# Kernel optimization log

Hardware: AMD Instinct MI355X
Metric: run time of the kernel (lower is better)

Reference implementation:

```python
import jax, jax.numpy as jnp
import numpy as np

EPS = 1e-5  # torch BatchNorm default eps


def _bn(x, g, b, axes):
    # Training-mode batch norm (biased variance, as torch uses for normalization)
    m = x.mean(axes, keepdims=True)
    v = x.var(axes, keepdims=True)
    sh = [1] * x.ndim
    sh[1] = x.shape[1]
    return (x - m) / jnp.sqrt(v + EPS) * g.reshape(sh) + b.reshape(sh)


def _conv2d(x, w, b, pad):
    y = jax.lax.conv_general_dilated(x, w, (1, 1), ((pad, pad), (pad, pad)),
                                     dimension_numbers=('NCHW', 'OIHW', 'NCHW'))
    return y + b.reshape(1, -1, 1, 1)


def _conv3d(x, w, b):
    # kernel (1,1,3), padding (0,0,1)
    y = jax.lax.conv_general_dilated(x, w, (1, 1, 1), ((0, 0), (0, 0), (1, 1)),
                                     dimension_numbers=('NCDHW', 'OIDHW', 'NCDHW'))
    return y + b.reshape(1, -1, 1, 1, 1)


def _block(x, w, b, g, be):
    return jax.nn.relu(_bn(_conv2d(x, w, b, 1), g, be, (0, 2, 3)))


def _pool(x):
    return jax.lax.reduce_window(x, -jnp.inf, jax.lax.max, (1, 1, 2, 2), (1, 1, 2, 2), 'VALID')


def _interp_axis(x, axis):
    # bilinear, align_corners=True, scale factor 2 along one axis
    n = x.shape[axis]
    out = 2 * n
    pos = jnp.linspace(0.0, n - 1.0, out)
    lo = jnp.floor(pos).astype(jnp.int32)
    hi = jnp.minimum(lo + 1, n - 1)
    w = (pos - lo).astype(x.dtype)
    sh = [1] * x.ndim
    sh[axis] = out
    w = w.reshape(sh)
    return jnp.take(x, lo, axis=axis) * (1 - w) + jnp.take(x, hi, axis=axis) * w


def _upsample(x):
    return _interp_axis(_interp_axis(x, 2), 3)


def _forward(x, tp_w1, tp_b1, tp_g1, tp_be1, tp_w2, tp_b2, tp_g2, tp_be2,
             range_w, doppler_w,
             enc1_w, enc1_b, enc1_g, enc1_be,
             enc2_w, enc2_b, enc2_g, enc2_be,
             enc3_w, enc3_b, enc3_g, enc3_be,
             dec3_w, dec3_b, dec3_g, dec3_be,
             dec2_w, dec2_b, dec2_g, dec2_be,
             dec1_w, dec1_b, dec1_g, dec1_be,
             out_w, out_b):
    # x: [B, RX, C, S, 2] -> [B, 2, RX, C, S]
    h = jnp.transpose(x, (0, 4, 1, 2, 3))
    h = jax.nn.relu(_bn(_conv3d(h, tp_w1, tp_b1), tp_g1, tp_be1, (0, 2, 3, 4)))
    h = jax.nn.relu(_bn(_conv3d(h, tp_w2, tp_b2), tp_g2, tp_be2, (0, 2, 3, 4)))
    h = jnp.transpose(h, (0, 2, 3, 4, 1)).sum(axis=1)  # sum over RX -> [B, C, S, 2]
    xr, xi = h[..., 0], h[..., 1]
    # Range DFT (quadruple loop in torch == two complex matmuls)
    Wr, Wi = range_w[..., 0], range_w[..., 1]  # [S, R]
    rr = jnp.einsum('bcs,sr->bcr', xr, Wr) - jnp.einsum('bcs,sr->bcr', xi, Wi)
    ri = jnp.einsum('bcs,sr->bcr', xr, Wi) + jnp.einsum('bcs,sr->bcr', xi, Wr)
    # Doppler DFT over chirps
    Dr, Di = doppler_w[..., 0], doppler_w[..., 1]  # [C, D]
    rdr = jnp.einsum('bcr,cd->bdr', rr, Dr) - jnp.einsum('bcr,cd->bdr', ri, Di)
    rdi = jnp.einsum('bcr,cd->bdr', rr, Di) + jnp.einsum('bcr,cd->bdr', ri, Dr)
    rd = jnp.stack([rdr, rdi], axis=1)  # [B, 2, D, R]
    # RadarNet U-Net
    e1 = _block(rd, enc1_w, enc1_b, enc1_g, enc1_be)
    p1 = _pool(e1)
    e2 = _block(p1, enc2_w, enc2_b, enc2_g, enc2_be)
    p2 = _pool(e2)
    e3 = _block(p2, enc3_w, enc3_b, enc3_g, enc3_be)
    d3 = _block(e3, dec3_w, dec3_b, dec3_g, dec3_be)
    u2 = _upsample(d3) + e2
    d2 = _block(u2, dec2_w, dec2_b, dec2_g, dec2_be)
    u1 = _upsample(d2) + e1
    d1 = _block(u1, dec1_w, dec1_b, dec1_g, dec1_be)
    out = jax.nn.sigmoid(_conv2d(d1, out_w, out_b, 0))
    return jnp.transpose(out, (0, 2, 3, 1))  # [B, D, R, 1]


def setup_inputs() -> dict:
    key = jax.random.key(0)
    ctr = [0]

    def rn(shape, scale=1.0):
        ctr[0] += 1
        return jax.random.normal(jax.random.fold_in(key, ctr[0]), shape, dtype=jnp.float32) * scale

    B, RX, C, S, D, R = 16, 4, 128, 256, 128, 256
    inp = {
        'x': rn((B, RX, C, S, 2)),
        'tp_w1': rn((8, 2, 1, 1, 3), 0.4), 'tp_b1': jnp.zeros(8), 'tp_g1': jnp.ones(8), 'tp_be1': jnp.zeros(8),
        'tp_w2': rn((2, 8, 1, 1, 3), 0.2), 'tp_b2': jnp.zeros(2), 'tp_g2': jnp.ones(2), 'tp_be2': jnp.zeros(2),
        'range_w': rn((S, R, 2)), 'doppler_w': rn((C, D, 2)),
        'enc1_w': rn((32, 2, 3, 3), 0.1), 'enc1_b': jnp.zeros(32), 'enc1_g': jnp.ones(32), 'enc1_be': jnp.zeros(32),
        'enc2_w': rn((64, 32, 3, 3), 0.05), 'enc2_b': jnp.zeros(64), 'enc2_g': jnp.ones(64), 'enc2_be': jnp.zeros(64),
        'enc3_w': rn((128, 64, 3, 3), 0.04), 'enc3_b': jnp.zeros(128), 'enc3_g': jnp.ones(128), 'enc3_be': jnp.zeros(128),
        'dec3_w': rn((64, 128, 3, 3), 0.03), 'dec3_b': jnp.zeros(64), 'dec3_g': jnp.ones(64), 'dec3_be': jnp.zeros(64),
        'dec2_w': rn((32, 64, 3, 3), 0.04), 'dec2_b': jnp.zeros(32), 'dec2_g': jnp.ones(32), 'dec2_be': jnp.zeros(32),
        'dec1_w': rn((16, 32, 3, 3), 0.05), 'dec1_b': jnp.zeros(16), 'dec1_g': jnp.ones(16), 'dec1_be': jnp.zeros(16),
        'out_w': rn((1, 16, 1, 1), 0.25), 'out_b': jnp.zeros(1),
    }
    return inp


def reference(x, tp_w1, tp_b1, tp_g1, tp_be1, tp_w2, tp_b2, tp_g2, tp_be2,
              range_w, doppler_w,
              enc1_w, enc1_b, enc1_g, enc1_be,
              enc2_w, enc2_b, enc2_g, enc2_be,
              enc3_w, enc3_b, enc3_g, enc3_be,
              dec3_w, dec3_b, dec3_g, dec3_be,
              dec2_w, dec2_b, dec2_g, dec2_be,
              dec1_w, dec1_b, dec1_g, dec1_be,
              out_w, out_b):
    return _forward(x, tp_w1, tp_b1, tp_g1, tp_be1, tp_w2, tp_b2, tp_g2, tp_be2,
                    range_w, doppler_w,
                    enc1_w, enc1_b, enc1_g, enc1_be,
                    enc2_w, enc2_b, enc2_g, enc2_be,
                    enc3_w, enc3_b, enc3_g, enc3_be,
                    dec3_w, dec3_b, dec3_g, dec3_be,
                    dec2_w, dec2_b, dec2_g, dec2_be,
                    dec1_w, dec1_b, dec1_g, dec1_be,
                    out_w, out_b)
```

## Files before the change

### kernel.cpp

```cpp
#include <hip/hip_runtime.h>
#include <cmath>

constexpr int Bn = 16, RXn = 4, Cn = 128, Sn = 256, Dn = 128, Rn = 256;

typedef __attribute__((ext_vector_type(8))) short bf16x8;
typedef __attribute__((ext_vector_type(4))) float f32x4;
typedef unsigned short u16;
typedef unsigned int u32;
typedef __attribute__((ext_vector_type(4))) u16 u16x4;
typedef __attribute__((ext_vector_type(8))) u16 u16x8;
typedef __attribute__((ext_vector_type(2))) u32 u32x2;
typedef __attribute__((ext_vector_type(4))) u32 u32x4;

__device__ __forceinline__ u16 f2bf(float f) {
  union { float f; u32 u; } v; v.f = f;
  const u32 r = v.u + 0x7FFFu + ((v.u >> 16) & 1u);
  return (u16)(r >> 16);
}
__device__ __forceinline__ float bf2f(u16 h) {
  union { u32 u; float f; } v; v.u = (u32)h << 16; return v.f;
}
__device__ __forceinline__ u32 cvtpk(float lo, float hi) {
  u32 r;
  asm("v_cvt_pk_bf16_f32 %0, %1, %2" : "=v"(r) : "v"(lo), "v"(hi));
  return r;
}
__device__ __forceinline__ void split2(float a, float b, u32& hi, u32& lo) {
  hi = cvtpk(a, b);
  union { u32 u; float f; } va, vb;
  va.u = hi << 16;
  vb.u = hi & 0xFFFF0000u;
  lo = cvtpk(a - va.f, b - vb.f);
}
__device__ __forceinline__ void ld8bf(const u16* __restrict__ p, float* v) {
  const u16x8 h = *(const u16x8*)p;
#pragma unroll
  for (int k = 0; k < 8; ++k) v[k] = bf2f(h[k]);
}

__device__ __forceinline__ void pack_seg(const float* __restrict__ w, u16* __restrict__ wpk,
                                         int CIN, int COUT, int gid, int gsz) {
  const int total = COUT * CIN * 9;
  const int chunks = CIN >> 5;
  for (int idx = gid; idx < total; idx += gsz) {
    const int j = idx & 7;
    const int l = (idx >> 3) & 63;
    const int rest = idx >> 9;
    const int t = rest % 9;
    const int rest2 = rest / 9;
    const int q = rest2 % chunks;
    const int mf = rest2 / chunks;
    const int co = mf * 16 + (l & 15);
    const int ci = q * 32 + ((l >> 4) << 3) + j;
    wpk[idx] = f2bf(w[((size_t)co * CIN + ci) * 9 + t]);
  }
}

__global__ __launch_bounds__(256) void k_pack_stats(
    const float* __restrict__ e2w, const float* __restrict__ e3w,
    const float* __restrict__ d3w, const float* __restrict__ d2w,
    const float* __restrict__ d1w,
    const float* __restrict__ range_w, const float* __restrict__ dopp_w,
    u16* __restrict__ p_e2, u16* __restrict__ p_e3,
    u16* __restrict__ p_d3, u16* __restrict__ p_d2,
    u16* __restrict__ p_d1,
    u16* __restrict__ A1h, u16* __restrict__ A1l,
    u16* __restrict__ A2h, u16* __restrict__ A2l,
    const float* __restrict__ x, const float* __restrict__ w1,
    float* __restrict__ part) {
  if (blockIdx.x < 128) {
    const int gid = blockIdx.x * 256 + threadIdx.x;
    const int gsz = 128 * 256;
    pack_seg(e2w, p_e2, 32, 64, gid, gsz);
    pack_seg(e3w, p_e3, 64, 128, gid, gsz);
    pack_seg(d3w, p_d3, 128, 64, gid, gsz);
    pack_seg(d2w, p_d2, 64, 32, gid, gsz);
    pack_seg(d1w, p_d1, 32, 16, gid, gsz);
    for (int idx = gid; idx < 512 * 512; idx += gsz) {
      const int m = idx >> 9, k = idx & 511;
      const int r = m >> 1, p = m & 1, s = k >> 1, q = k & 1;
      const float Wr = range_w[((size_t)s * Rn + r) * 2 + 0];
      const float Wi = range_w[((size_t)s * Rn + r) * 2 + 1];
      const float v = (p == 0) ? ((q == 0) ? Wr : -Wi) : ((q == 0) ? Wi : Wr);
      const u16 h = f2bf(v);
      A1h[idx] = h;
      A1l[idx] = f2bf(v - bf2f(h));
    }
    for (int idx = gid; idx < 256 * 256; idx += gsz) {
      const int m = idx >> 8, k = idx & 255;
      const int d = m >> 1, p = m & 1, c = k >> 1, q = k & 1;
      const float Dr = dopp_w[((size_t)c * Dn + d) * 2 + 0];
      const float Di = dopp_w[((size_t)c * Dn + d) * 2 + 1];
      const float v = (p == 0) ? ((q == 0) ? Dr : -Di) : ((q == 0) ? Di : Dr);
      const u16 h = f2bf(v);
      A2h[idx] = h;
      A2l[idx] = f2bf(v - bf2f(h));
    }
    return;
  }
  const int bx = blockIdx.x - 128;
  __shared__ float w1s[48];
  __shared__ float red8[8][4][2];
  const int t = threadIdx.x;
  if (t < 48) w1s[t] = w1[t];
  __syncthreads();
  float s1[8], s2[8];
#pragma unroll
  for (int o = 0; o < 8; ++o) { s1[o] = 0.f; s2[o] = 0.f; }
  for (int row = bx; row < Bn * RXn * Cn; row += 1024) {
    const float* xr = x + (size_t)row * Sn * 2;
    const float2 cc = *(const float2*)&xr[2 * t];
    const float2 mm = (t > 0) ? *(const float2*)&xr[2 * t - 2] : make_float2(0.f, 0.f);
    const float2 pp = (t < Sn - 1) ? *(const float2*)&xr[2 * t + 2] : make_float2(0.f, 0.f);
#pragma unroll
    for (int o = 0; o < 8; ++o) {
      const float* w = &w1s[o * 6];
      float h = w[0] * mm.x + w[1] * cc.x + w[2] * pp.x + w[3] * mm.y + w[4] * cc.y + w[5] * pp.y;
      s1[o] += h; s2[o] += h * h;
    }
  }
  const int lane = t & 63, wv = t >> 6;
#pragma unroll
  for (int o = 0; o < 8; ++o) {
    float v1 = s1[o], v2 = s2[o];
#pragma unroll
    for (int off = 32; off; off >>= 1) { v1 += __shfl_down(v1, off); v2 += __shfl_down(v2, off); }
    if (lane == 0) { red8[o][wv][0] = v1; red8[o][wv][1] = v2; }
  }
  __syncthreads();
  if (t < 8) {
    const float a1 = red8[t][0][0] + red8[t][1][0] + red8[t][2][0] + red8[t][3][0];
    const float a2 = red8[t][0][1] + red8[t][1][1] + red8[t][2][1] + red8[t][3][1];
    part[((size_t)t * 1024 + bx) * 2 + 0] = a1;
    part[((size_t)t * 1024 + bx) * 2 + 1] = a2;
  }
}

__global__ __launch_bounds__(256) void k_finalize(const float* __restrict__ part, int npart,
                                                  float n, const float* __restrict__ g,
                                                  const float* __restrict__ be,
                                                  float* __restrict__ stats) {
  const int co = blockIdx.x, t = threadIdx.x;
  __shared__ float r1[256], r2[256];
  float s1 = 0.f, s2 = 0.f;
  for (int i = t; i < npart; i += 256) {
    s1 += part[((size_t)co * npart + i) * 2 + 0];
    s2 += part[((size_t)co * npart + i) * 2 + 1];
  }
  r1[t] = s1; r2[t] = s2;
  __syncthreads();
  for (int off = 128; off; off >>= 1) {
    if (t < off) { r1[t] += r1[t + off]; r2[t] += r2[t + off]; }
    __syncthreads();
  }
  if (t == 0) {
    const float mean = r1[0] / n;
    const float var  = fmaxf(r2[0] / n - mean * mean, 0.f);
    const float inv  = rsqrtf(var + 1e-5f);
    const float sc   = inv * g[co];
    stats[2 * co + 0] = sc;
    stats[2 * co + 1] = be[co] - mean * sc;
  }
}

__global__ __launch_bounds__(256) void k_tp_fused2(const float* __restrict__ x,
                                                   const float* __restrict__ w1,
                                                   const float* __restrict__ st1,
                                                   const float* __restrict__ w2,
                                                   u32* __restrict__ h2p,
                                                   float* __restrict__ part) {
  __shared__ float a1[8][Sn + 2];
  __shared__ float w1s[48], w2s[48], st[16];
  __shared__ float red2s[2][4][2];
  const int t = threadIdx.x;
  const int row = blockIdx.x;
  if (t < 48) { w1s[t] = w1[t]; w2s[t] = w2[t]; }
  if (t < 16) st[t] = st1[t];
  __syncthreads();
  const float* xr = x + (size_t)row * Sn * 2;
  const float2 cc = *(const float2*)&xr[2 * t];
  const float2 mm = (t > 0) ? *(const float2*)&xr[2 * t - 2] : make_float2(0.f, 0.f);
  const float2 pp = (t < Sn - 1) ? *(const float2*)&xr[2 * t + 2] : make_float2(0.f, 0.f);
#pragma unroll
  for (int o = 0; o < 8; ++o) {
    const float* w = &w1s[o * 6];
    float h = w[0] * mm.x + w[1] * cc.x + w[2] * pp.x + w[3] * mm.y + w[4] * cc.y + w[5] * pp.y;
    float v = fmaf(h, st[2 * o], st[2 * o + 1]);
    a1[o][1 + t] = v > 0.f ? v : 0.f;
    if (t == 0) { a1[o][0] = 0.f; a1[o][Sn + 1] = 0.f; }
  }
  __syncthreads();
  float h2v[2];
#pragma unroll
  for (int j = 0; j < 2; ++j) {
    float acc = 0.f;
#pragma unroll
    for (int o = 0; o < 8; ++o) {
      const float* w = &w2s[j * 24 + o * 3];
      acc += w[0] * a1[o][t] + w[1] * a1[o][t + 1] + w[2] * a1[o][t + 2];
    }
    h2v[j] = acc;
  }
  h2p[(size_t)row * Sn + t] = cvtpk(h2v[0], h2v[1]);
  const int lane = t & 63, wv = t >> 6;
#pragma unroll
  for (int j = 0; j < 2; ++j) {
    float v1 = h2v[j], v2 = h2v[j] * h2v[j];
#pragma unroll
    for (int off = 32; off; off >>= 1) { v1 += __shfl_down(v1, off); v2 += __shfl_down(v2, off); }
    if (lane == 0) { red2s[j][wv][0] = v1; red2s[j][wv][1] = v2; }
  }
  __syncthreads();
  if (t < 2) {
    const float a1s = red2s[t][0][0] + red2s[t][1][0] + red2s[t][2][0] + red2s[t][3][0];
    const float a2s = red2s[t][0][1] + red2s[t][1][1] + red2s[t][2][1] + red2s[t][3][1];
    part[((size_t)t * gridDim.x + row) * 2 + 0] = a1s;
    part[((size_t)t * gridDim.x + row) * 2 + 1] = a2s;
  }
}

__global__ __launch_bounds__(256) void k_prep(const u32* __restrict__ h2p,
                                              const float* __restrict__ st2,
                                              u32* __restrict__ B1h32,
                                              u32* __restrict__ B1l32) {
  const int row = blockIdx.x;
  const int s = threadIdx.x;
  const int b = row >> 7, c = row & (Cn - 1);
  const float sc0 = st2[0], sh0 = st2[1], sc1 = st2[2], sh1 = st2[3];
  float xr = 0.f, xi = 0.f;
#pragma unroll
  for (int rx = 0; rx < RXn; ++rx) {
    const u32 v = h2p[(((size_t)b * RXn + rx) * Cn + c) * Sn + s];
    const float vr = bf2f((u16)(v & 0xFFFFu));
    const float vi = bf2f((u16)(v >> 16));
    xr += fmaxf(fmaf(vr, sc0, sh0), 0.f);
    xi += fmaxf(fmaf(vi, sc1, sh1), 0.f);
  }
  u32 hi, lo;
  split2(xr, xi, hi, lo);
  B1h32[(size_t)row * 256 + s] = hi;
  B1l32[(size_t)row * 256 + s] = lo;
}

template <int M, int N, int K, int STORE>
__global__ __launch_bounds__(256) void k_gemm_split(const u16* __restrict__ Ah,
                                                    const u16* __restrict__ Al,
                                                    const u16* __restrict__ Bh,
                                                    const u16* __restrict__ Bl,
                                                    u32* __restrict__ out0,
                                                    u32* __restrict__ out1) {
  __shared__ __align__(16) u16 lah[32 * 40], lal[32 * 40];
  __shared__ __align__(16) u16 lbh[64 * 40], lbl[64 * 40];
  const int tid = threadIdx.x;
  const int lane = tid & 63, wid = tid >> 6;
  const int wm = wid >> 1, wn = wid & 1;
  const int l15 = lane & 15, lg = lane >> 4;
  const int m0 = blockIdx.x * 32, n0 = blockIdx.y * 64;
  f32x4 acc[2];
  acc[0] = (f32x4){0.f, 0.f, 0.f, 0.f};
  acc[1] = (f32x4){0.f, 0.f, 0.f, 0.f};
  const int arow = tid >> 3, ak = (tid & 7) * 4;
  const int brow = tid >> 2, bk = (tid & 3) * 8;
  for (int k0 = 0; k0 < K; k0 += 32) {
    *(u16x4*)&lah[arow * 40 + ak] = *(const u16x4*)&Ah[(size_t)(m0 + arow) * K + k0 + ak];
    *(u16x4*)&lal[arow * 40 + ak] = *(const u16x4*)&Al[(size_t)(m0 + arow) * K + k0 + ak];
    *(u16x8*)&lbh[brow * 40 + bk] = *(const u16x8*)&Bh[(size_t)(n0 + brow) * K + k0 + bk];
    *(u16x8*)&lbl[brow * 40 + bk] = *(const u16x8*)&Bl[(size_t)(n0 + brow) * K + k0 + bk];
    __syncthreads();
    const bf16x8 ah = *(const bf16x8*)&lah[(wm * 16 + l15) * 40 + lg * 8];
    const bf16x8 al = *(const bf16x8*)&lal[(wm * 16 + l15) * 40 + lg * 8];
#pragma unroll
    for (int f = 0; f < 2; ++f) {
      const bf16x8 bh = *(const bf16x8*)&lbh[(wn * 32 + f * 16 + l15) * 40 + lg * 8];
      const bf16x8 bl = *(const bf16x8*)&lbl[(wn * 32 + f * 16 + l15) * 40 + lg * 8];
      acc[f] = __builtin_amdgcn_mfma_f32_16x16x32_bf16(ah, bh, acc[f], 0, 0, 0);
      acc[f] = __builtin_amdgcn_mfma_f32_16x16x32_bf16(ah, bl, acc[f], 0, 0, 0);
      acc[f] = __builtin_amdgcn_mfma_f32_16x16x32_bf16(al, bh, acc[f], 0, 0, 0);
    }
    __syncthreads();
  }
  const int mb = m0 + wm * 16 + lg * 4;
#pragma unroll
  for (int f = 0; f < 2; ++f) {
    const int n = n0 + wn * 32 + f * 16 + l15;
    if (STORE == 0) {
      const int b = n >> 7, c = n & 127;
#pragma unroll
      for (int pair = 0; pair < 2; ++pair) {
        const int r = (mb >> 1) + pair;
        u32 hi, lo;
        split2(acc[f][2 * pair], acc[f][2 * pair + 1], hi, lo);
        const size_t idx = ((size_t)b * 256 + r) * 128 + c;
        out0[idx] = hi;
        out1[idx] = lo;
      }
    } else {
      const int b = n >> 8, r = n & 255;
#pragma unroll
      for (int pair = 0; pair < 2; ++pair) {
        const int d = (mb >> 1) + pair;
        out0[((size_t)b * 128 + d) * 256 + r] = cvtpk(acc[f][2 * pair], acc[f][2 * pair + 1]);
      }
    }
  }
}

template <int CIN, int COUT, int H, int W, int TH, int TW, int MW, int NW,
          int WAVES_M, int WAVES_N, int MODE>
__global__ __launch_bounds__(256) void k_conv_mfma(const u16* __restrict__ in,
                                                   const u16* __restrict__ wpk,
                                                   const float* __restrict__ in_stats,
                                                   const u16* __restrict__ in2,
                                                   const float* __restrict__ in2_stats,
                                                   u16* __restrict__ out,
                                                   float* __restrict__ part) {
  constexpr int COG = WAVES_M * MW * 16;
  constexpr int CHUNKS = CIN / 32;
  constexpr int NFROW = TW / 16;
  constexpr int XROWS = TH + 2, XCOLS = TW + 2;
  static_assert(WAVES_M * WAVES_N == 4, "waves");
  static_assert(WAVES_N * NW * 16 == TH * TW, "pixel cover");
  __shared__ __align__(16) u16 xs[XROWS * XCOLS * 40];
  __shared__ float red1[WAVES_N][COG], red2[WAVES_N][COG];
  __shared__ __align__(16) float sst1[2 * CIN];
  __shared__ __align__(16) float sst2[(MODE == 3) ? 2 * CIN : 4];
  const int tid = threadIdx.x;
  const int lane = tid & 63;
  const int wid = tid >> 6;
  const int wave_m = wid / WAVES_N;
  const int wave_n = wid % WAVES_N;
  const int l15 = lane & 15, lg = lane >> 4;
  constexpr int TILES_W = W / TW;
  const int tile = blockIdx.x;
  const int tw = tile % TILES_W, th = tile / TILES_W;
  const int h0 = th * TH, w0 = tw * TW;
  const int cog = blockIdx.y, b = blockIdx.z;
  for (int i = tid; i < 2 * CIN; i += 256) sst1[i] = in_stats[i];
  if (MODE == 3)
    for (int i = tid; i < 2 * CIN; i += 256) sst2[i] = in2_stats[i];
  __syncthreads();
  f32x4 acc[MW][NW];
#pragma unroll
  for (int m = 0; m < MW; ++m)
#pragma unroll
    for (int f = 0; f < NW; ++f) acc[m][f] = (f32x4){0.f, 0.f, 0.f, 0.f};

  for (int q = 0; q < CHUNKS; ++q) {
    for (int i = tid; i < XROWS * XCOLS * 4; i += 256) {
      const int ci0 = (i & 3) * 8;
      const int pix = i >> 2;
      const int col = pix % XCOLS;
      const int row = pix / XCOLS;
      const int gh = h0 + row - 1, gw = w0 + col - 1;
      const int cch = q * 32 + ci0;
      u32x4 enc = (u32x4){0u, 0u, 0u, 0u};
      if (gh >= 0 && gh < H && gw >= 0 && gw < W) {
        float vv[8];
        float sc[8], sh[8];
#pragma unroll
        for (int k = 0; k < 4; ++k) {
          const float4 qq = *(const float4*)&sst1[2 * cch + 4 * k];
          sc[2 * k] = qq.x; sh[2 * k] = qq.y; sc[2 * k + 1] = qq.z; sh[2 * k + 1] = qq.w;
        }
        if (MODE == 1) {
          float tv[8];
          ld8bf(&in[(((size_t)b * H + gh) * W + gw) * CIN + cch], tv);
#pragma unroll
          for (int k = 0; k < 8; ++k) vv[k] = fmaxf(fmaf(tv[k], sc[k], sh[k]), 0.f);
        } else if (MODE == 2) {
          const size_t rs = (size_t)(2 * W) * CIN;
          const u16* pb = &in[(((size_t)b * 2 * H + 2 * gh) * (2 * W) + 2 * gw) * CIN + cch];
          float tp[4][8];
          ld8bf(pb, tp[0]);
          ld8bf(pb + CIN, tp[1]);
          ld8bf(pb + rs, tp[2]);
          ld8bf(pb + rs + CIN, tp[3]);
#pragma unroll
          for (int k = 0; k < 8; ++k) {
            const float mx = fmaxf(fmaxf(tp[0][k], tp[1][k]), fmaxf(tp[2][k], tp[3][k]));
            vv[k] = fmaxf(fmaf(mx, sc[k], sh[k]), 0.f);
          }
        } else {
          constexpr int Hi2 = H / 2, Wi2 = W / 2;
          constexpr float steph = (float)(Hi2 - 1) / (float)(H - 1);
          constexpr float stepw = (float)(Wi2 - 1) / (float)(W - 1);
          const float ph = (float)gh * steph;
          const int hlo = (int)ph;
          const int hhi = (hlo + 1 < Hi2) ? hlo + 1 : Hi2 - 1;
          const float fh = ph - (float)hlo;
          const float pw = (float)gw * stepw;
          const int wl = (int)pw;
          const int wh = (wl + 1 < Wi2) ? wl + 1 : Wi2 - 1;
          const float fw = pw - (float)wl;
          const float w00 = (1.f - fh) * (1.f - fw), w01 = (1.f - fh) * fw;
          const float w10 = fh * (1.f - fw), w11 = fh * fw;
          const u16* dbase = &in[(size_t)b * Hi2 * Wi2 * CIN + cch];
          float tp[4][8];
          ld8bf(dbase + ((size_t)hlo * Wi2 + wl) * CIN, tp[0]);
          ld8bf(dbase + ((size_t)hlo * Wi2 + wh) * CIN, tp[1]);
          ld8bf(dbase + ((size_t)hhi * Wi2 + wl) * CIN, tp[2]);
          ld8bf(dbase + ((size_t)hhi * Wi2 + wh) * CIN, tp[3]);
          float ec[8], es[8];
#pragma unroll
          for (int k = 0; k < 4; ++k) {
            const float4 qq = *(const float4*)&sst2[2 * cch + 4 * k];
            ec[2 * k] = qq.x; es[2 * k] = qq.y; ec[2 * k + 1] = qq.z; es[2 * k + 1] = qq.w;
          }
          float ev[8];
          ld8bf(&in2[(((size_t)b * H + gh) * W + gw) * CIN + cch], ev);
#pragma unroll
          for (int k = 0; k < 8; ++k) {
            const float a = fmaxf(fmaf(tp[0][k], sc[k], sh[k]), 0.f);
            const float bb = fmaxf(fmaf(tp[1][k], sc[k], sh[k]), 0.f);
            const float cc = fmaxf(fmaf(tp[2][k], sc[k], sh[k]), 0.f);
            const float dd = fmaxf(fmaf(tp[3][k], sc[k], sh[k]), 0.f);
            vv[k] = w00 * a + w01 * bb + w10 * cc + w11 * dd
                  + fmaxf(fmaf(ev[k], ec[k], es[k]), 0.f);
          }
        }
#pragma unroll
        for (int j = 0; j < 4; ++j) enc[j] = cvtpk(vv[2 * j], vv[2 * j + 1]);
      }
      *(u32x4*)&xs[(row * XCOLS + col) * 40 + ci0] = enc;
    }
    __syncthreads();
#pragma unroll
    for (int t = 0; t < 9; ++t) {
      const int ky = t / 3, kx = t % 3;
      bf16x8 afr[MW];
#pragma unroll
      for (int m = 0; m < MW; ++m) {
        const int mfg = cog * (COG / 16) + wave_m * MW + m;
        afr[m] = *(const bf16x8*)&wpk[((((size_t)mfg * CHUNKS + q) * 9 + t) * 64 + lane) * 8];
      }
      bf16x8 bfr[NW];
#pragma unroll
      for (int f = 0; f < NW; ++f) {
        const int nf = wave_n * NW + f;
        const int r = nf / NFROW;
        const int cseg = (nf % NFROW) * 16;
        bfr[f] = *(const bf16x8*)&xs[((r + ky) * XCOLS + (cseg + l15 + kx)) * 40 + lg * 8];
      }
#pragma unroll
      for (int m = 0; m < MW; ++m)
#pragma unroll
        for (int f = 0; f < NW; ++f)
          acc[m][f] = __builtin_amdgcn_mfma_f32_16x16x32_bf16(afr[m], bfr[f], acc[m][f], 0, 0, 0);
    }
    __syncthreads();
  }

#pragma unroll
  for (int m = 0; m < MW; ++m) {
    const int cobase = cog * COG + (wave_m * MW + m) * 16 + lg * 4;
#pragma unroll
    for (int f = 0; f < NW; ++f) {
      const int nf = wave_n * NW + f;
      const int r = nf / NFROW;
      const int cseg = (nf % NFROW) * 16;
      u16* op = out + (((size_t)b * H + h0 + r) * W + (w0 + cseg + l15)) * COUT + cobase;
      u32x2 ov;
      ov[0] = cvtpk(acc[m][f][0], acc[m][f][1]);
      ov[1] = cvtpk(acc[m][f][2], acc[m][f][3]);
      *(u32x2*)op = ov;
    }
  }
#pragma unroll
  for (int m = 0; m < MW; ++m)
#pragma unroll
    for (int reg = 0; reg < 4; ++reg) {
      float s1 = 0.f, s2 = 0.f;
#pragma unroll
      for (int f = 0; f < NW; ++f) { const float v = acc[m][f][reg]; s1 += v; s2 += v * v; }
#pragma unroll
      for (int off = 1; off < 16; off <<= 1) { s1 += __shfl_xor(s1, off); s2 += __shfl_xor(s2, off); }
      if (l15 == 0) {
        const int ch = (wave_m * MW + m) * 16 + lg * 4 + reg;
        red1[wave_n][ch] = s1; red2[wave_n][ch] = s2;
      }
    }
  __syncthreads();
  if (tid < COG) {
    float s1 = 0.f, s2 = 0.f;
#pragma unroll
    for (int wn = 0; wn < WAVES_N; ++wn) { s1 += red1[wn][tid]; s2 += red2[wn][tid]; }
    const int npart = gridDim.x * gridDim.z;
    const int pidx = blockIdx.z * gridDim.x + blockIdx.x;
    part[((size_t)(cog * COG + tid) * npart + pidx) * 2 + 0] = s1;
    part[((size_t)(cog * COG + tid) * npart + pidx) * 2 + 1] = s2;
  }
}

__global__ __launch_bounds__(256) void k_conv1(const u32* __restrict__ in,
                                               const float* __restrict__ wgt,
                                               u16* __restrict__ out,
                                               float* __restrict__ part) {
  constexpr int H = 128, W = 256, TW = 64, TH = 16, COG = 16, COUT = 32;
  const int tid = threadIdx.x;
  const int tile = blockIdx.x;
  const int tw = tile & 3, th = tile >> 2;
  const int cog = blockIdx.y, b = blockIdx.z;
  const int ty = tid >> 4;
  const int wofs = (tid & 15) * 4;
  const int h0 = th * TH, w0t = tw * TW;
  __shared__ float xs0[TH + 2][TW + 3], xs1[TH + 2][TW + 3];
  __shared__ float ws[2][COG][12];
  __shared__ float redp[4][COG], redq[4][COG];
  for (int i = tid; i < 2 * COG * 9; i += 256) {
    const int tap = i % 9, rest = i / 9;
    const int ci = rest & 1, co = rest >> 1;
    ws[ci][co][tap] = wgt[((size_t)(cog * COG + co) * 2 + ci) * 9 + tap];
  }
  for (int i = tid; i < (TH + 2) * (TW + 2); i += 256) {
    const int col = i % (TW + 2), row = i / (TW + 2);
    const int gh = h0 + row - 1, gw = w0t + col - 1;
    float v0 = 0.f, v1 = 0.f;
    if (gh >= 0 && gh < H && gw >= 0 && gw < W) {
      const u32 v = in[((size_t)b * H + gh) * W + gw];
      v0 = bf2f((u16)(v & 0xFFFFu));
      v1 = bf2f((u16)(v >> 16));
    }
    xs0[row][col] = v0; xs1[row][col] = v1;
  }
  __syncthreads();
  float acc[4][COG];
#pragma unroll
  for (int px = 0; px < 4; ++px)
#pragma unroll
    for (int co = 0; co < COG; ++co) acc[px][co] = 0.f;
#pragma unroll
  for (int ci = 0; ci < 2; ++ci) {
    float xrow[3][6];
#pragma unroll
    for (int ky = 0; ky < 3; ++ky)
#pragma unroll
      for (int j = 0; j < 6; ++j)
        xrow[ky][j] = ci ? xs1[ty + ky][wofs + j] : xs0[ty + ky][wofs + j];
#pragma unroll
    for (int co = 0; co < COG; ++co) {
      const float4 wq0 = *(const float4*)&ws[ci][co][0];
      const float4 wq1 = *(const float4*)&ws[ci][co][4];
      const float  w8 = ws[ci][co][8];
      const float wv[9] = {wq0.x, wq0.y, wq0.z, wq0.w, wq1.x, wq1.y, wq1.z, wq1.w, w8};
#pragma unroll
      for (int ky = 0; ky < 3; ++ky)
#pragma unroll
        for (int kx = 0; kx < 3; ++kx)
#pragma unroll
          for (int px = 0; px < 4; ++px)
            acc[px][co] = fmaf(xrow[ky][px + kx], wv[ky * 3 + kx], acc[px][co]);
    }
  }
#pragma unroll
  for (int px = 0; px < 4; ++px) {
    u16* op = out + (((size_t)b * H + h0 + ty) * W + (w0t + wofs + px)) * COUT + cog * COG;
    u32x4 ov;
    ov[0] = cvtpk(acc[px][0], acc[px][1]);
    ov[1] = cvtpk(acc[px][2], acc[px][3]);
    ov[2] = cvtpk(acc[px][4], acc[px][5]);
    ov[3] = cvtpk(acc[px][6], acc[px][7]);
    *(u32x4*)&op[0] = ov;
    u32x4 ov2;
    ov2[0] = cvtpk(acc[px][8], acc[px][9]);
    ov2[1] = cvtpk(acc[px][10], acc[px][11]);
    ov2[2] = cvtpk(acc[px][12], acc[px][13]);
    ov2[3] = cvtpk(acc[px][14], acc[px][15]);
    *(u32x4*)&op[8] = ov2;
  }
  const int lane = tid & 63, wid = tid >> 6;
#pragma unroll
  for (int co = 0; co < COG; ++co) {
    float v1 = 0.f, v2 = 0.f;
#pragma unroll
    for (int px = 0; px < 4; ++px) { v1 += acc[px][co]; v2 += acc[px][co] * acc[px][co]; }
#pragma unroll
    for (int off = 32; off; off >>= 1) { v1 += __shfl_down(v1, off); v2 += __shfl_down(v2, off); }
    if (lane == 0) { redp[wid][co] = v1; redq[wid][co] = v2; }
  }
  __syncthreads();
  if (tid < COG) {
    const int npart = gridDim.x * gridDim.z;
    const int pidx = blockIdx.z * gridDim.x + blockIdx.x;
    part[((size_t)(cog * COG + tid) * npart + pidx) * 2 + 0] = redp[0][tid] + redp[1][tid] + redp[2][tid] + redp[3][tid];
    part[((size_t)(cog * COG + tid) * npart + pidx) * 2 + 1] = redq[0][tid] + redq[1][tid] + redq[2][tid] + redq[3][tid];
  }
}

__global__ __launch_bounds__(256) void k_out_bn(const u16* __restrict__ d1,
                                                const float* __restrict__ st,
                                                const float* __restrict__ ow,
                                                const float* __restrict__ ob,
                                                float* __restrict__ out) {
  const size_t i = (size_t)blockIdx.x * 256 + threadIdx.x;
  const size_t total = (size_t)Bn * Dn * Rn;
  if (i >= total) return;
  const u16* p = d1 + i * 16;
  float v[16];
  ld8bf(p, v);
  ld8bf(p + 8, v + 8);
  float acc = ob[0];
#pragma unroll
  for (int k = 0; k < 16; ++k) {
    const float2 q = *(const float2*)&st[2 * k];
    acc += fmaxf(fmaf(v[k], q.x, q.y), 0.f) * ow[k];
  }
  out[i] = 1.f / (1.f + expf(-acc));
}

extern "C" void kernel_launch(void* const* d_in, const int* in_sizes, int n_in,
                              void* d_out, int out_size, void* d_ws, size_t ws_size,
                              hipStream_t stream) {
  (void)in_sizes; (void)n_in; (void)out_size; (void)ws_size;
  const float* x       = (const float*)d_in[0];
  const float* tp_w1   = (const float*)d_in[1];
  const float* tp_g1   = (const float*)d_in[3];
  const float* tp_be1  = (const float*)d_in[4];
  const float* tp_w2   = (const float*)d_in[5];
  const float* tp_g2   = (const float*)d_in[7];
  const float* tp_be2  = (const float*)d_in[8];
  const float* range_w = (const float*)d_in[9];
  const float* dopp_w  = (const float*)d_in[10];
  const float* e1w = (const float*)d_in[11]; const float* e1g = (const float*)d_in[13]; const float* e1b = (const float*)d_in[14];
  const float* e2w = (const float*)d_in[15]; const float* e2g = (const float*)d_in[17]; const float* e2b = (const float*)d_in[18];
  const float* e3w = (const float*)d_in[19]; const float* e3g = (const float*)d_in[21]; const float* e3b = (const float*)d_in[22];
  const float* d3w = (const float*)d_in[23]; const float* d3g = (const float*)d_in[25]; const float* d3b = (const float*)d_in[26];
  const float* d2w = (const float*)d_in[27]; const float* d2g = (const float*)d_in[29]; const float* d2b = (const float*)d_in[30];
  const float* d1w = (const float*)d_in[31]; const float* d1g = (const float*)d_in[33]; const float* d1b = (const float*)d_in[34];
  const float* out_w = (const float*)d_in[35];
  const float* out_b = (const float*)d_in[36];
  float* outp = (float*)d_out;

  float* W  = (float*)d_ws;
  u16* Ae1  = (u16*)W;
  float* Bx = W + 16777216;
  u16* Ce2  = (u16*)(W + 33554432);
  u16* Ee3  = (u16*)(W + 41943040);
  u16* Fd3  = (u16*)(W + 46137344);
  float* part  = W + 48234496;
  float* stats = part + 262144;
  u16* wpk_e2 = (u16*)(stats + 1024);
  u16* wpk_e3 = wpk_e2 + 18432;
  u16* wpk_d3 = wpk_e3 + 73728;
  u16* wpk_d2 = wpk_d3 + 73728;
  u16* wpk_d1 = wpk_d2 + 18432;
  u16* A1h = wpk_d1 + 4608;
  u16* A1l = A1h + 262144;
  u16* A2h = A1l + 262144;
  u16* A2l = A2h + 65536;
  u16* B1h = A2l + 65536;
  u16* B1l = B1h + 1048576;
  u16* B2h = B1l + 1048576;
  u16* B2l = B2h + 1048576;

  u32* h2p = (u32*)Bx;
  u32* rd  = (u32*)(Bx + 2097152 + 65536);
  u16* d1  = (u16*)Bx;

  float* st_tp1 = stats;
  float* st_tp2 = stats + 16;
  float* st_e1  = stats + 32;
  float* st_e2  = stats + 96;
  float* st_e3  = stats + 224;
  float* st_d3  = stats + 480;
  float* st_d2  = stats + 608;
  float* st_d1  = stats + 672;

  const float Ntp = 2097152.f;

  k_pack_stats<<<1152, 256, 0, stream>>>(e2w, e3w, d3w, d2w, d1w, range_w, dopp_w,
                                         wpk_e2, wpk_e3, wpk_d3, wpk_d2, wpk_d1,
                                         A1h, A1l, A2h, A2l,
                                         x, tp_w1, part);
  k_finalize<<<8, 256, 0, stream>>>(part, 1024, Ntp, tp_g1, tp_be1, st_tp1);
  k_tp_fused2<<<Bn * RXn * Cn, 256, 0, stream>>>(x, tp_w1, st_tp1, tp_w2, h2p, part);
  k_finalize<<<2, 256, 0, stream>>>(part, Bn * RXn * Cn, Ntp, tp_g2, tp_be2, st_tp2);

  k_prep<<<Bn * Cn, 256, 0, stream>>>(h2p, st_tp2, (u32*)B1h, (u32*)B1l);
  k_gemm_split<512, 2048, 512, 0><<<dim3(16, 32), 256, 0, stream>>>(
      A1h, A1l, B1h, B1l, (u32*)B2h, (u32*)B2l);
  k_gemm_split<256, 4096, 256, 1><<<dim3(8, 64), 256, 0, stream>>>(
      A2h, A2l, B2h, B2l, rd, nullptr);

  k_conv1<<<dim3(32, 2, Bn), 256, 0, stream>>>(rd, e1w, Ae1, part);
  k_finalize<<<32, 256, 0, stream>>>(part, 512, 524288.f, e1g, e1b, st_e1);
  k_conv_mfma<32, 64, 64, 128, 8, 32, 2, 8, 2, 2, 2><<<dim3(32, 1, Bn), 256, 0, stream>>>(
      Ae1, wpk_e2, st_e1, nullptr, nullptr, Ce2, part);
  k_finalize<<<64, 256, 0, stream>>>(part, 512, 131072.f, e2g, e2b, st_e2);
  k_conv_mfma<64, 128, 32, 64, 4, 16, 1, 4, 4, 1, 2><<<dim3(32, 2, Bn), 256, 0, stream>>>(
      Ce2, wpk_e3, st_e2, nullptr, nullptr, Ee3, part);
  k_finalize<<<128, 256, 0, stream>>>(part, 512, 32768.f, e3g, e3b, st_e3);
  k_conv_mfma<128, 64, 32, 64, 4, 16, 1, 4, 4, 1, 1><<<dim3(32, 1, Bn), 256, 0, stream>>>(
      Ee3, wpk_d3, st_e3, nullptr, nullptr, Fd3, part);
  k_finalize<<<64, 256, 0, stream>>>(part, 512, 32768.f, d3g, d3b, st_d3);
  k_conv_mfma<64, 32, 64, 128, 8, 32, 1, 8, 2, 2, 3><<<dim3(32, 1, Bn), 256, 0, stream>>>(
      Fd3, wpk_d2, st_d3, Ce2, st_e2, Ee3, part);
  k_finalize<<<32, 256, 0, stream>>>(part, 512, 131072.f, d2g, d2b, st_d2);
  k_conv_mfma<32, 16, 128, 256, 8, 32, 1, 4, 1, 4, 3><<<dim3(128, 1, Bn), 256, 0, stream>>>(
      Ee3, wpk_d1, st_d2, Ae1, st_e1, d1, part);
  k_finalize<<<16, 256, 0, stream>>>(part, 2048, 524288.f, d1g, d1b, st_d1);
  k_out_bn<<<2048, 256, 0, stream>>>(d1, st_d1, out_w, out_b, outp);
}
```

Before: 223.5 us.

## Replace per-layer BN finalize kernels with sharded atomic sums computed in consumers

Batch-norm partial statistics are now accumulated with atomicAdd into 16 sharded sum buffers instead of per-block partial arrays. The separate finalize launches for the second time-pulse conv and the encoder/decoder layers are removed, and each consuming kernel derives scale/shift from the shards at startup. This removes about seven small kernel launches and their serialization. In exchange it adds atomic traffic, redundant stats computation in every consuming block, and a buffer zeroing step, and atomics make the summation order nondeterministic.

```diff
diff --git a/kernel.cpp b/kernel.cpp
--- a/kernel.cpp
+++ b/kernel.cpp
@@ -2,6 +2,11 @@
 #include <cmath>
 
 constexpr int Bn = 16, RXn = 4, Cn = 128, Sn = 256, Dn = 128, Rn = 256;
+
+constexpr int NSH = 16;
+constexpr int SUMSZ = 676;
+constexpr int OFF_TP2 = 0, OFF_E1 = 4, OFF_E2 = 68, OFF_E3 = 196;
+constexpr int OFF_D3 = 452, OFF_D2 = 580, OFF_D1 = 644;
 
 typedef __attribute__((ext_vector_type(8))) short bf16x8;
 typedef __attribute__((ext_vector_type(4))) float f32x4;
@@ -36,6 +41,24 @@
   const u16x8 h = *(const u16x8*)p;
 #pragma unroll
   for (int k = 0; k < 8; ++k) v[k] = bf2f(h[k]);
+}
+
+__device__ __forceinline__ void stats_from_sums(const float* __restrict__ sums,
+                                                int ch, float n,
+                                                const float* __restrict__ g,
+                                                const float* __restrict__ be,
+                                                float& sc, float& sh) {
+  float s1 = 0.f, s2 = 0.f;
+#pragma unroll
+  for (int s = 0; s < NSH; ++s) {
+    const float2 q = *(const float2*)&sums[s * SUMSZ + 2 * ch];
+    s1 += q.x; s2 += q.y;
+  }
+  const float mean = s1 / n;
+  const float var  = fmaxf(s2 / n - mean * mean, 0.f);
+  const float inv  = rsqrtf(var + 1e-5f);
+  sc = inv * g[ch];
+  sh = be[ch] - mean * sc;
 }
 
 __device__ __forceinline__ void pack_seg(const float* __restrict__ w, u16* __restrict__ wpk,
@@ -67,10 +90,11 @@
     u16* __restrict__ A1h, u16* __restrict__ A1l,
     u16* __restrict__ A2h, u16* __restrict__ A2l,
     const float* __restrict__ x, const float* __restrict__ w1,
-    float* __restrict__ part) {
+    float* __restrict__ part, float* __restrict__ sums) {
   if (blockIdx.x < 128) {
     const int gid = blockIdx.x * 256 + threadIdx.x;
     const int gsz = 128 * 256;
+    for (int idx = gid; idx < NSH * SUMSZ; idx += gsz) sums[idx] = 0.f;
     pack_seg(e2w, p_e2, 32, 64, gid, gsz);
     pack_seg(e3w, p_e3, 64, 128, gid, gsz);
     pack_seg(d3w, p_d3, 128, 64, gid, gsz);
@@ -168,7 +192,7 @@
                                                    const float* __restrict__ st1,
                                                    const float* __restrict__ w2,
                                                    u32* __restrict__ h2p,
-                                                   float* __restrict__ part) {
+                                                   float* __restrict__ sums) {
   __shared__ float a1[8][Sn + 2];
   __shared__ float w1s[48], w2s[48], st[16];
   __shared__ float red2s[2][4][2];
@@ -214,19 +238,25 @@
   if (t < 2) {
     const float a1s = red2s[t][0][0] + red2s[t][1][0] + red2s[t][2][0] + red2s[t][3][0];
     const float a2s = red2s[t][0][1] + red2s[t][1][1] + red2s[t][2][1] + red2s[t][3][1];
-    part[((size_t)t * gridDim.x + row) * 2 + 0] = a1s;
-    part[((size_t)t * gridDim.x + row) * 2 + 1] = a2s;
+    float* dst = sums + (size_t)(blockIdx.x & (NSH - 1)) * SUMSZ + OFF_TP2 + 2 * t;
+    atomicAdd(&dst[0], a1s);
+    atomicAdd(&dst[1], a2s);
   }
 }
 
 __global__ __launch_bounds__(256) void k_prep(const u32* __restrict__ h2p,
-                                              const float* __restrict__ st2,
+                                              const float* __restrict__ sums,
+                                              const float* __restrict__ g2,
+                                              const float* __restrict__ be2,
                                               u32* __restrict__ B1h32,
                                               u32* __restrict__ B1l32) {
   const int row = blockIdx.x;
   const int s = threadIdx.x;
   const int b = row >> 7, c = row & (Cn - 1);
-  const float sc0 = st2[0], sh0 = st2[1], sc1 = st2[2], sh1 = st2[3];
+  const float Ntp = 2097152.f;
+  float sc0, sh0, sc1, sh1;
+  stats_from_sums(sums + OFF_TP2, 0, Ntp, g2, be2, sc0, sh0);
+  stats_from_sums(sums + OFF_TP2, 1, Ntp, g2, be2, sc1, sh1);
   float xr = 0.f, xi = 0.f;
 #pragma unroll
   for (int rx = 0; rx < RXn; ++rx) {
@@ -309,11 +339,17 @@
           int WAVES_M, int WAVES_N, int MODE>
 __global__ __launch_bounds__(256) void k_conv_mfma(const u16* __restrict__ in,
                                                    const u16* __restrict__ wpk,
-                                                   const float* __restrict__ in_stats,
+                                                   const float* __restrict__ sums_in,
+                                                   const float* __restrict__ g_in,
+                                                   const float* __restrict__ be_in,
+                                                   float n_in,
                                                    const u16* __restrict__ in2,
-                                                   const float* __restrict__ in2_stats,
+                                                   const float* __restrict__ sums_in2,
+                                                   const float* __restrict__ g2_in,
+                                                   const float* __restrict__ be2_in,
+                                                   float n2_in,
                                                    u16* __restrict__ out,
-                                                   float* __restrict__ part) {
+                                                   float* __restrict__ sums_out) {
   constexpr int COG = WAVES_M * MW * 16;
   constexpr int CHUNKS = CIN / 32;
   constexpr int NFROW = TW / 16;
@@ -335,9 +371,17 @@
   const int tw = tile % TILES_W, th = tile / TILES_W;
   const int h0 = th * TH, w0 = tw * TW;
   const int cog = blockIdx.y, b = blockIdx.z;
-  for (int i = tid; i < 2 * CIN; i += 256) sst1[i] = in_stats[i];
+  for (int ch = tid; ch < CIN; ch += 256) {
+    float sc, sh;
+    stats_from_sums(sums_in, ch, n_in, g_in, be_in, sc, sh);
+    sst1[2 * ch] = sc; sst1[2 * ch + 1] = sh;
+  }
   if (MODE == 3)
-    for (int i = tid; i < 2 * CIN; i += 256) sst2[i] = in2_stats[i];
+    for (int ch = tid; ch < CIN; ch += 256) {
+      float sc, sh;
+      stats_from_sums(sums_in2, ch, n2_in, g2_in, be2_in, sc, sh);
+      sst2[2 * ch] = sc; sst2[2 * ch + 1] = sh;
+    }
   __syncthreads();
   f32x4 acc[MW][NW];
 #pragma unroll
@@ -484,17 +528,17 @@
     float s1 = 0.f, s2 = 0.f;
 #pragma unroll
     for (int wn = 0; wn < WAVES_N; ++wn) { s1 += red1[wn][tid]; s2 += red2[wn][tid]; }
-    const int npart = gridDim.x * gridDim.z;
-    const int pidx = blockIdx.z * gridDim.x + blockIdx.x;
-    part[((size_t)(cog * COG + tid) * npart + pidx) * 2 + 0] = s1;
-    part[((size_t)(cog * COG + tid) * npart + pidx) * 2 + 1] = s2;
+    const int shard = (blockIdx.z * gridDim.x + blockIdx.x) & (NSH - 1);
+    float* dst = sums_out + (size_t)shard * SUMSZ + 2 * (cog * COG + tid);
+    atomicAdd(&dst[0], s1);
+    atomicAdd(&dst[1], s2);
   }
 }
 
 __global__ __launch_bounds__(256) void k_conv1(const u32* __restrict__ in,
                                                const float* __restrict__ wgt,
                                                u16* __restrict__ out,
-                                               float* __restrict__ part) {
+                                               float* __restrict__ sums_out) {
   constexpr int H = 128, W = 256, TW = 64, TH = 16, COG = 16, COUT = 32;
   const int tid = threadIdx.x;
   const int tile = blockIdx.x;
@@ -579,19 +623,29 @@
   }
   __syncthreads();
   if (tid < COG) {
-    const int npart = gridDim.x * gridDim.z;
-    const int pidx = blockIdx.z * gridDim.x + blockIdx.x;
-    part[((size_t)(cog * COG + tid) * npart + pidx) * 2 + 0] = redp[0][tid] + redp[1][tid] + redp[2][tid] + redp[3][tid];
-    part[((size_t)(cog * COG + tid) * npart + pidx) * 2 + 1] = redq[0][tid] + redq[1][tid] + redq[2][tid] + redq[3][tid];
+    const int shard = (blockIdx.z * gridDim.x + blockIdx.x) & (NSH - 1);
+    float* dst = sums_out + (size_t)shard * SUMSZ + 2 * (cog * COG + tid);
+    atomicAdd(&dst[0], redp[0][tid] + redp[1][tid] + redp[2][tid] + redp[3][tid]);
+    atomicAdd(&dst[1], redq[0][tid] + redq[1][tid] + redq[2][tid] + redq[3][tid]);
   }
 }
 
 __global__ __launch_bounds__(256) void k_out_bn(const u16* __restrict__ d1,
-                                                const float* __restrict__ st,
+                                                const float* __restrict__ sums_d1,
+                                                const float* __restrict__ g,
+                                                const float* __restrict__ be,
                                                 const float* __restrict__ ow,
                                                 const float* __restrict__ ob,
                                                 float* __restrict__ out) {
-  const size_t i = (size_t)blockIdx.x * 256 + threadIdx.x;
+  __shared__ float st[32];
+  const int t = threadIdx.x;
+  if (t < 16) {
+    float sc, sh;
+    stats_from_sums(sums_d1, t, 524288.f, g, be, sc, sh);
+    st[2 * t] = sc; st[2 * t + 1] = sh;
+  }
+  __syncthreads();
+  const size_t i = (size_t)blockIdx.x * 256 + t;
   const size_t total = (size_t)Bn * Dn * Rn;
   if (i >= total) return;
   const u16* p = d1 + i * 16;
@@ -638,7 +692,9 @@
   u16* Fd3  = (u16*)(W + 46137344);
   float* part  = W + 48234496;
   float* stats = part + 262144;
-  u16* wpk_e2 = (u16*)(stats + 1024);
+  float* st_tp1 = stats;
+  float* sums   = stats + 16;
+  u16* wpk_e2 = (u16*)(sums + NSH * SUMSZ);
   u16* wpk_e3 = wpk_e2 + 18432;
   u16* wpk_d3 = wpk_e3 + 73728;
   u16* wpk_d2 = wpk_d3 + 73728;
@@ -656,47 +712,36 @@
   u32* rd  = (u32*)(Bx + 2097152 + 65536);
   u16* d1  = (u16*)Bx;
 
-  float* st_tp1 = stats;
-  float* st_tp2 = stats + 16;
-  float* st_e1  = stats + 32;
-  float* st_e2  = stats + 96;
-  float* st_e3  = stats + 224;
-  float* st_d3  = stats + 480;
-  float* st_d2  = stats + 608;
-  float* st_d1  = stats + 672;
-
   const float Ntp = 2097152.f;
 
   k_pack_stats<<<1152, 256, 0, stream>>>(e2w, e3w, d3w, d2w, d1w, range_w, dopp_w,
                                          wpk_e2, wpk_e3, wpk_d3, wpk_d2, wpk_d1,
                                          A1h, A1l, A2h, A2l,
-                                         x, tp_w1, part);
+                                         x, tp_w1, part, sums);
   k_finalize<<<8, 256, 0, stream>>>(part, 1024, Ntp, tp_g1, tp_be1, st_tp1);
-  k_tp_fused2<<<Bn * RXn * Cn, 256, 0, stream>>>(x, tp_w1, st_tp1, tp_w2, h2p, part);
-  k_finalize<<<2, 256, 0, stream>>>(part, Bn * RXn * Cn, Ntp, tp_g2, tp_be2, st_tp2);
-
-  k_prep<<<Bn * Cn, 256, 0, stream>>>(h2p, st_tp2, (u32*)B1h, (u32*)B1l);
+  k_tp_fused2<<<Bn * RXn * Cn, 256, 0, stream>>>(x, tp_w1, st_tp1, tp_w2, h2p, sums);
+
+  k_prep<<<Bn * Cn, 256, 0, stream>>>(h2p, sums, tp_g2, tp_be2, (u32*)B1h, (u32*)B1l);
   k_gemm_split<512, 2048, 512, 0><<<dim3(16, 32), 256, 0, stream>>>(
       A1h, A1l, B1h, B1l, (u32*)B2h, (u32*)B2l);
   k_gemm_split<256, 4096, 256, 1><<<dim3(8, 64), 256, 0, stream>>>(
       A2h, A2l, B2h, B2l, rd, nullptr);
 
-  k_conv1<<<dim3(32, 2, Bn), 256, 0, stream>>>(rd, e1w, Ae1, part);
-  k_finalize<<<32, 256, 0, stream>>>(part, 512, 524288.f, e1g, e1b, st_e1);
+  k_conv1<<<dim3(32, 2, Bn), 256, 0, stream>>>(rd, e1w, Ae1, sums + OFF_E1);
   k_conv_mfma<32, 64, 64, 128, 8, 32, 2, 8, 2, 2, 2><<<dim3(32, 1, Bn), 256, 0, stream>>>(
-      Ae1, wpk_e2, st_e1, nullptr, nullptr, Ce2, part);
-  k_finalize<<<64, 256, 0, stream>>>(part, 512, 131072.f, e2g, e2b, st_e2);
+      Ae1, wpk_e2, sums + OFF_E1, e1g, e1b, 524288.f,
+      nullptr, nullptr, nullptr, nullptr, 0.f, Ce2, sums + OFF_E2);
   k_conv_mfma<64, 128, 32, 64, 4, 16, 1, 4, 4, 1, 2><<<dim3(32, 2, Bn), 256, 0, stream>>>(
-      Ce2, wpk_e3, st_e2, nullptr, nullptr, Ee3, part);
-  k_finalize<<<128, 256, 0, stream>>>(part, 512, 32768.f, e3g, e3b, st_e3);
+      Ce2, wpk_e3, sums + OFF_E2, e2g, e2b, 131072.f,
+      nullptr, nullptr, nullptr, nullptr, 0.f, Ee3, sums + OFF_E3);
   k_conv_mfma<128, 64, 32, 64, 4, 16, 1, 4, 4, 1, 1><<<dim3(32, 1, Bn), 256, 0, stream>>>(
-      Ee3, wpk_d3, st_e3, nullptr, nullptr, Fd3, part);
-  k_finalize<<<64, 256, 0, stream>>>(part, 512, 32768.f, d3g, d3b, st_d3);
+      Ee3, wpk_d3, sums + OFF_E3, e3g, e3b, 32768.f,
+      nullptr, nullptr, nullptr, nullptr, 0.f, Fd3, sums + OFF_D3);
   k_conv_mfma<64, 32, 64, 128, 8, 32, 1, 8, 2, 2, 3><<<dim3(32, 1, Bn), 256, 0, stream>>>(
-      Fd3, wpk_d2, st_d3, Ce2, st_e2, Ee3, part);
-  k_finalize<<<32, 256, 0, stream>>>(part, 512, 131072.f, d2g, d2b, st_d2);
+      Fd3, wpk_d2, sums + OFF_D3, d3g, d3b, 32768.f,
+      Ce2, sums + OFF_E2, e2g, e2b, 131072.f, Ee3, sums + OFF_D2);
   k_conv_mfma<32, 16, 128, 256, 8, 32, 1, 4, 1, 4, 3><<<dim3(128, 1, Bn), 256, 0, stream>>>(
-      Ee3, wpk_d1, st_d2, Ae1, st_e1, d1, part);
-  k_finalize<<<16, 256, 0, stream>>>(part, 2048, 524288.f, d1g, d1b, st_d1);
-  k_out_bn<<<2048, 256, 0, stream>>>(d1, st_d1, out_w, out_b, outp);
-}
+      Ee3, wpk_d1, sums + OFF_D2, d2g, d2b, 131072.f,
+      Ae1, sums + OFF_E1, e1g, e1b, 524288.f, d1, sums + OFF_D1);
+  k_out_bn<<<2048, 256, 0, stream>>>(d1, sums + OFF_D1, d1g, d1b, out_w, out_b, outp);
+}
```

After: 231.9 us. +3.8%, slower.
